# Performance work log

Hardware: AMD Instinct MI355X
Metric: run time of the kernel (lower is better)

## Reference

```python
import jax, jax.numpy as jnp
import numpy as np

DN = ('NCHW', 'OIHW', 'NCHW')
B, C, H, W = 4, 64, 256, 256
MIP = 8          # max(8, C // 32)
RED = C // 16    # CBAM reduced channels
PS = 8           # FSAS patch size


def conv2d(x, w, padding=0, groups=1):
    return jax.lax.conv_general_dilated(
        x, w, (1, 1), [(padding, padding), (padding, padding)],
        dimension_numbers=DN, feature_group_count=groups)


def bn_eval(x, g, b, eps=1e-5):
    # BatchNorm with init running stats (mean=0, var=1), eval mode
    return x / jnp.sqrt(1.0 + eps) * g[None, :, None, None] + b[None, :, None, None]


def h_swish(x):
    return x * jnp.clip(x + 3.0, 0.0, 6.0) / 6.0


def setup_inputs() -> dict:
    key = jax.random.key(0)
    ks = jax.random.split(key, 12)
    s = 0.05
    d = {
        'x': jax.random.normal(ks[0], (B, C, H, W), jnp.float32),
        # CoordAttention
        'ca_conv1_w': jax.random.normal(ks[1], (MIP, C, 1, 1), jnp.float32) * s,
        'ca_conv1_b': jnp.zeros((MIP,), jnp.float32),
        'ca_bn_g': jnp.ones((MIP,), jnp.float32),
        'ca_bn_b': jnp.zeros((MIP,), jnp.float32),
        'ca_convh_w': jax.random.normal(ks[2], (C, MIP, 1, 1), jnp.float32) * s,
        'ca_convh_b': jnp.zeros((C,), jnp.float32),
        'ca_convw_w': jax.random.normal(ks[3], (C, MIP, 1, 1), jnp.float32) * s,
        'ca_convw_b': jnp.zeros((C,), jnp.float32),
        # FSAS (bias=False)
        'fsas_hidden_w': jax.random.normal(ks[4], (6 * C, C, 1, 1), jnp.float32) * s,
        'fsas_dw_w': jax.random.normal(ks[5], (6 * C, 1, 3, 3), jnp.float32) * s,
        'fsas_proj_w': jax.random.normal(ks[6], (C, 2 * C, 1, 1), jnp.float32) * s,
        'ln_w': jnp.ones((2 * C,), jnp.float32),
        'ln_b': jnp.zeros((2 * C,), jnp.float32),
        # Fusion
        'fus_conv1_w': jax.random.normal(ks[7], (2 * C, 2 * C, 3, 3), jnp.float32) * s,
        'fus_bn1_g': jnp.ones((2 * C,), jnp.float32),
        'fus_bn1_b': jnp.zeros((2 * C,), jnp.float32),
        'fus_conv2_w': jax.random.normal(ks[8], (C, 2 * C, 1, 1), jnp.float32) * s,
        'fus_bn2_g': jnp.ones((C,), jnp.float32),
        'fus_bn2_b': jnp.zeros((C,), jnp.float32),
        # CBAM
        'cbam_mlp1_w': jax.random.normal(ks[9], (RED, C, 1, 1), jnp.float32) * s,
        'cbam_mlp2_w': jax.random.normal(ks[10], (C, RED, 1, 1), jnp.float32) * s,
        'cbam_sa_w': jax.random.normal(ks[11], (1, 2, 7, 7), jnp.float32) * s,
        'residual_scale': jnp.float32(0.1),
    }
    return d


def _forward(x, ca_conv1_w, ca_conv1_b, ca_bn_g, ca_bn_b, ca_convh_w, ca_convh_b,
             ca_convw_w, ca_convw_b, fsas_hidden_w, fsas_dw_w, fsas_proj_w, ln_w, ln_b,
             fus_conv1_w, fus_bn1_g, fus_bn1_b, fus_conv2_w, fus_bn2_g, fus_bn2_b,
             cbam_mlp1_w, cbam_mlp2_w, cbam_sa_w, residual_scale):
    b, c, h, w = x.shape
    c2 = 2 * c

    # ---- CoordAttention branch ----
    xh = jnp.mean(x, axis=3, keepdims=True)                       # [B,C,H,1]
    xw = jnp.mean(x, axis=2, keepdims=True).transpose(0, 1, 3, 2)  # [B,C,W,1]
    y = jnp.concatenate([xh, xw], axis=2)                          # [B,C,H+W,1]
    y = conv2d(y, ca_conv1_w) + ca_conv1_b[None, :, None, None]
    y = h_swish(bn_eval(y, ca_bn_g, ca_bn_b))
    yh, yw = y[:, :, :h], y[:, :, h:]
    yw = yw.transpose(0, 1, 3, 2)
    a_h = jax.nn.sigmoid(conv2d(yh, ca_convh_w) + ca_convh_b[None, :, None, None])
    a_w = jax.nn.sigmoid(conv2d(yw, ca_convw_w) + ca_convw_b[None, :, None, None])
    ca_out = x * a_h * a_w

    # ---- FSAS branch ----
    hid = conv2d(x, fsas_hidden_w)                                 # [B,6C,H,W]
    hid = conv2d(hid, fsas_dw_w, padding=1, groups=6 * c)          # depthwise 3x3
    q, k, v = jnp.split(hid, 3, axis=1)                            # each [B,2C,H,W]

    def patch(t):  # [B,2C,H,W] -> [B,2C,H/8,W/8,8,8]
        return t.reshape(b, c2, h // PS, PS, w // PS, PS).transpose(0, 1, 2, 4, 3, 5)

    qf = jnp.fft.rfft2(patch(q))
    kf = jnp.fft.rfft2(patch(k))
    o = jnp.fft.irfft2(qf * kf, s=(PS, PS))
    o = o.transpose(0, 1, 2, 4, 3, 5).reshape(b, c2, h, w)

    # WithBias LayerNorm over channel dim (per pixel)
    mu = jnp.mean(o, axis=1, keepdims=True)
    var = jnp.var(o, axis=1, keepdims=True)
    on = (o - mu) / jnp.sqrt(var + 1e-5) * ln_w[None, :, None, None] + ln_b[None, :, None, None]
    fsas_out = conv2d(v * on, fsas_proj_w)                         # [B,C,H,W]

    # ---- Fusion ----
    f = conv2d(jnp.concatenate([ca_out, fsas_out], axis=1), fus_conv1_w, padding=1)
    f = jax.nn.gelu(bn_eval(f, fus_bn1_g, fus_bn1_b), approximate=False)
    f = bn_eval(conv2d(f, fus_conv2_w), fus_bn2_g, fus_bn2_b)

    z = x + residual_scale * f

    # ---- CBAM ----
    avg = jnp.mean(z, axis=(2, 3), keepdims=True)
    mx = jnp.max(z, axis=(2, 3), keepdims=True)

    def mlp(t):
        return conv2d(jax.nn.relu(conv2d(t, cbam_mlp1_w)), cbam_mlp2_w)

    z = z * jax.nn.sigmoid(mlp(avg) + mlp(mx))
    sa = jnp.concatenate([jnp.mean(z, axis=1, keepdims=True),
                          jnp.max(z, axis=1, keepdims=True)], axis=1)
    z = z * jax.nn.sigmoid(conv2d(sa, cbam_sa_w, padding=3))
    return jax.nn.gelu(z, approximate=False)


def reference(x, ca_conv1_w, ca_conv1_b, ca_bn_g, ca_bn_b, ca_convh_w, ca_convh_b,
              ca_convw_w, ca_convw_b, fsas_hidden_w, fsas_dw_w, fsas_proj_w, ln_w, ln_b,
              fus_conv1_w, fus_bn1_g, fus_bn1_b, fus_conv2_w, fus_bn2_g, fus_bn2_b,
              cbam_mlp1_w, cbam_mlp2_w, cbam_sa_w, residual_scale):
    return _forward(x, ca_conv1_w, ca_conv1_b, ca_bn_g, ca_bn_b, ca_convh_w, ca_convh_b,
                    ca_convw_w, ca_convw_b, fsas_hidden_w, fsas_dw_w, fsas_proj_w, ln_w, ln_b,
                    fus_conv1_w, fus_bn1_g, fus_bn1_b, fus_conv2_w, fus_bn2_g, fus_bn2_b,
                    cbam_mlp1_w, cbam_mlp2_w, cbam_sa_w, residual_scale)
```

## Files before the change

kernel.cpp:

```cpp
#include <hip/hip_runtime.h>
#include <math.h>

#define B_ 4
#define C_ 64
#define C2_ 128
#define C6_ 384
#define H_ 256
#define Wd_ 256
#define HW_ 65536
#define MIP_ 8
#define BNINV 0.9999950000374994f

typedef short bf16x8 __attribute__((ext_vector_type(8)));
typedef float f32x4 __attribute__((ext_vector_type(4)));
typedef unsigned short u16x8 __attribute__((ext_vector_type(8)));
typedef unsigned short u16x4 __attribute__((ext_vector_type(4)));
typedef unsigned int   u32x4 __attribute__((ext_vector_type(4)));

__device__ __forceinline__ float sigm(float x){ return 1.f/(1.f+expf(-x)); }
__device__ __forceinline__ float gelu_f(float x){ return 0.5f*x*(1.f+erff(x*0.7071067811865476f)); }
__device__ __forceinline__ unsigned short bfrnd(float f){
  unsigned u = __float_as_uint(f);
  unsigned r = u + 0x7FFFu + ((u>>16)&1u);
  return (unsigned short)(r>>16);
}
__device__ __forceinline__ float bf2f(unsigned short s){
  return __uint_as_float(((unsigned)s)<<16);
}

__global__ void k_rowmean(const float* __restrict__ x, float* __restrict__ xh){
  int row = blockIdx.x*4 + (threadIdx.x>>6);
  int lane = threadIdx.x & 63;
  const float* p = x + (size_t)row*Wd_;
  float s = p[lane]+p[lane+64]+p[lane+128]+p[lane+192];
  #pragma unroll
  for(int off=32; off>0; off>>=1) s += __shfl_down(s, off, 64);
  if(lane==0) xh[row] = s*(1.f/Wd_);
}

__global__ void k_colmean(const float* __restrict__ x, float* __restrict__ xw){
  int idx = blockIdx.x*256 + threadIdx.x;
  int w = idx & 255; int bc = idx >> 8;
  const float* p = x + (size_t)bc*HW_ + w;
  float s = 0.f;
  for(int h=0;h<H_;h++) s += p[h*Wd_];
  xw[idx] = s*(1.f/H_);
}

__global__ void k_ca_t(const float* __restrict__ xh, const float* __restrict__ xw,
                       const float* __restrict__ w1, const float* __restrict__ b1,
                       const float* __restrict__ bng, const float* __restrict__ bnb,
                       float* __restrict__ t){
  int idx = blockIdx.x*256 + threadIdx.x;
  int p = idx & 511; int m = (idx>>9)&7; int b = idx>>12;
  float acc = b1[m];
  #pragma unroll 8
  for(int c=0;c<C_;c++){
    float yv = (p<256) ? xh[(b*C_+c)*256 + p] : xw[(b*C_+c)*256 + (p-256)];
    acc += w1[m*C_+c]*yv;
  }
  float v = acc*BNINV*bng[m] + bnb[m];
  t[idx] = v * fminf(fmaxf(v+3.f,0.f),6.f)*(1.f/6.f);
}

__global__ void k_ca_a(const float* __restrict__ t,
                       const float* __restrict__ wh, const float* __restrict__ bh,
                       const float* __restrict__ ww, const float* __restrict__ bw,
                       float* __restrict__ ah, float* __restrict__ aw){
  int idx = blockIdx.x*256 + threadIdx.x;
  int p = idx & 511; int co = (idx>>9)&63; int b = idx>>15;
  bool isH = (p<256);
  const float* wm = isH ? wh : ww;
  float acc = isH ? bh[co] : bw[co];
  #pragma unroll
  for(int m=0;m<MIP_;m++) acc += wm[co*MIP_+m]*t[(b*MIP_+m)*512+p];
  float s = sigm(acc);
  if(isH) ah[(b*C_+co)*256+p] = s; else aw[(b*C_+co)*256+(p-256)] = s;
}

__global__ void __launch_bounds__(256) k_xprep(const float* __restrict__ x, unsigned short* __restrict__ xb){
  __shared__ float sm[64][65];
  int tid = threadIdx.x;
  int img = blockIdx.x >> 10;
  int p0 = (blockIdx.x & 1023)*64;
  int lane = tid & 63, wq = tid >> 6;
  #pragma unroll
  for(int cc=0; cc<16; ++cc){
    int c = cc*4 + wq;
    sm[c][lane] = x[(size_t)(img*C_+c)*HW_ + p0 + lane];
  }
  __syncthreads();
  int pl = tid >> 2;
  int c0 = (tid & 3) * 16;
  u16x8 lo, hi;
  #pragma unroll
  for(int i=0;i<8;i++)  lo[i] = bfrnd(sm[c0+i][pl]);
  #pragma unroll
  for(int i=0;i<8;i++)  hi[i] = bfrnd(sm[c0+8+i][pl]);
  unsigned short* dst = xb + ((size_t)img*HW_ + p0 + pl)*64 + c0;
  *(u16x8*)(dst)     = lo;
  *(u16x8*)(dst + 8) = hi;
}

__global__ void k_wprep(const float* __restrict__ w, unsigned short* __restrict__ wbt){
  int t = blockIdx.x*256 + threadIdx.x;
  const float* src = w + (size_t)t*9;
  int oc = t >> 7, ic = t & 127;
  #pragma unroll
  for(int tap=0; tap<9; ++tap)
    wbt[(size_t)(tap*128+oc)*128 + ic] = bfrnd(src[tap]);
}

__global__ void k_wprep2(const float* __restrict__ pw, const float* __restrict__ w2,
                         const float* __restrict__ hw, unsigned short* __restrict__ pwb,
                         unsigned short* __restrict__ w2b, unsigned short* __restrict__ wb1){
  int t = blockIdx.x*256 + threadIdx.x;
  if(t < 8192){ pwb[t] = bfrnd(pw[t]); w2b[t] = bfrnd(w2[t]); }
  wb1[t] = bfrnd(hw[t]);
}

__global__ void __launch_bounds__(256) k_hid0_mfma(const unsigned short* __restrict__ xb,
                                                   const unsigned short* __restrict__ wb1,
                                                   unsigned short* __restrict__ hid0b){
  int tid = threadIdx.x;
  int lane = tid & 63, wid = tid >> 6;
  int l15 = lane & 15, lk = lane >> 4;
  int p0 = blockIdx.x*128 + wid*32;
  int oc0 = blockIdx.y*96;
  f32x4 acc[6][2];
  #pragma unroll
  for(int m=0;m<6;m++)
    #pragma unroll
    for(int n=0;n<2;n++) acc[m][n] = (f32x4)0.f;
  #pragma unroll
  for(int kk=0; kk<2; ++kk){
    bf16x8 bfr[2];
    #pragma unroll
    for(int n=0;n<2;n++)
      bfr[n] = *(const bf16x8*)(xb + (size_t)(p0 + n*16 + l15)*64 + kk*32 + lk*8);
    #pragma unroll
    for(int m=0;m<6;m++){
      bf16x8 af = *(const bf16x8*)(wb1 + (size_t)(oc0 + m*16 + l15)*64 + kk*32 + lk*8);
      #pragma unroll
      for(int n=0;n<2;n++)
        acc[m][n] = __builtin_amdgcn_mfma_f32_16x16x32_bf16(af, bfr[n], acc[m][n], 0,0,0);
    }
  }
  #pragma unroll
  for(int n=0;n<2;n++){
    int p = p0 + n*16 + l15;
    #pragma unroll
    for(int m=0;m<6;m++){
      u16x4 v;
      #pragma unroll
      for(int r=0;r<4;r++) v[r] = bfrnd(acc[m][n][r]);
      *(u16x4*)(hid0b + (size_t)p*384 + oc0 + m*16 + lk*4) = v;
    }
  }
}

__global__ void __launch_bounds__(256) k_dw_bf(const unsigned short* __restrict__ hid0b,
                                               const float* __restrict__ wd,
                                               unsigned short* __restrict__ hidb){
  int tid = threadIdx.x;
  int cg = tid & 15;
  int tg = tid >> 4;
  int p0 = blockIdx.x*64;
  int h  = p0 >> 8;
  int w0 = (p0 & 255) + tg*4;
  int chb = blockIdx.y*128 + cg*8;

  float wreg[72];
  {
    const f32x4* wsrc = (const f32x4*)(wd + (size_t)chb*9);
    #pragma unroll
    for(int i=0;i<18;i++){
      f32x4 v = wsrc[i];
      wreg[4*i+0]=v[0]; wreg[4*i+1]=v[1]; wreg[4*i+2]=v[2]; wreg[4*i+3]=v[3];
    }
  }
  float acc[4][8];
  #pragma unroll
  for(int px=0;px<4;px++)
    #pragma unroll
    for(int e=0;e<8;e++) acc[px][e] = 0.f;

  #pragma unroll
  for(int ky=0; ky<3; ++ky){
    int hh = h + ky - 1;
    if((unsigned)hh >= 256u) continue;
    float row[6][8];
    #pragma unroll
    for(int c6=0; c6<6; ++c6){
      int ww = w0 + c6 - 1;
      u16x8 v8 = {0,0,0,0,0,0,0,0};
      if((unsigned)ww < 256u)
        v8 = *(const u16x8*)(hid0b + (size_t)(hh*256+ww)*384 + chb);
      #pragma unroll
      for(int e=0;e<8;e++) row[c6][e] = bf2f(v8[e]);
    }
    #pragma unroll
    for(int kx=0; kx<3; ++kx){
      #pragma unroll
      for(int px=0; px<4; ++px){
        #pragma unroll
        for(int e=0;e<8;e++)
          acc[px][e] += row[px+kx][e] * wreg[e*9 + ky*3 + kx];
      }
    }
  }
  #pragma unroll
  for(int px=0; px<4; ++px){
    u16x8 o8;
    #pragma unroll
    for(int e=0;e<8;e++) o8[e] = bfrnd(acc[px][e]);
    *(u16x8*)(hidb + (size_t)(p0 + tg*4 + px)*384 + chb) = o8;
  }
}

__global__ void __launch_bounds__(256) k_circ_bf(const unsigned short* __restrict__ hidb,
                                                 unsigned short* __restrict__ ob){
  __shared__ __align__(16) unsigned short lq[2][64][128];
  __shared__ __align__(16) unsigned short lkk[2][64][128];
  int tid = threadIdx.x;
  #pragma unroll
  for(int it=0; it<8; ++it){
    int s = it*256 + tid;
    int which = s >> 10, rem = s & 1023;
    int pix = rem >> 4, cg = rem & 15;
    int gp = blockIdx.x*2 + which;
    int ph = gp >> 5, pw = gp & 31;
    size_t pg = (size_t)((ph*8 + (pix>>3))*256 + pw*8 + (pix&7));
    *(u16x8*)&lq[which][pix][cg*8]  = *(const u16x8*)(hidb + pg*384 + cg*8);
    *(u16x8*)&lkk[which][pix][cg*8] = *(const u16x8*)(hidb + pg*384 + 128 + cg*8);
  }
  __syncthreads();
  int which = tid >> 7, c = tid & 127;
  float kr[64];
  #pragma unroll
  for(int pix=0;pix<64;pix++) kr[pix] = bf2f(lkk[which][pix][c]);
  float outv[64];
  #pragma unroll
  for(int t2=0;t2<64;t2++) outv[t2] = 0.f;
  #pragma unroll
  for(int u=0;u<8;u++){
    #pragma unroll
    for(int v=0;v<8;v++){
      float qv = bf2f(lq[which][u*8+v][c]);
      #pragma unroll
      for(int i=0;i<8;i++){
        #pragma unroll
        for(int j=0;j<8;j++)
          outv[i*8+j] += qv * kr[((i-u)&7)*8 + ((j-v)&7)];
      }
    }
  }
  __syncthreads();
  #pragma unroll
  for(int t2=0;t2<64;t2++) lq[which][t2][c] = bfrnd(outv[t2]);
  __syncthreads();
  #pragma unroll
  for(int it=0; it<8; ++it){
    int s = it*256 + tid;
    int which2 = s >> 10, rem = s & 1023;
    int pix = rem >> 4, cg = rem & 15;
    int gp = blockIdx.x*2 + which2;
    int ph = gp >> 5, pw = gp & 31;
    size_t pg = (size_t)((ph*8 + (pix>>3))*256 + pw*8 + (pix&7));
    *(u16x8*)(ob + pg*128 + cg*8) = *(u16x8*)&lq[which2][pix][cg*8];
  }
}

__global__ void __launch_bounds__(256) k_proj_mfma(const unsigned short* __restrict__ ob,
                      const unsigned short* __restrict__ hidb,
                      const float* __restrict__ lnw, const float* __restrict__ lnb,
                      const unsigned short* __restrict__ pwb, unsigned short* __restrict__ catb){
  __shared__ unsigned int lds32[256*64];
  int tid = threadIdx.x;
  int lane = tid & 63, wid = tid >> 6;
  int p0 = blockIdx.x*256;
  {
    int p = p0 + tid;
    u16x8 o8[16];
    #pragma unroll
    for(int g=0; g<16; ++g) o8[g] = *(const u16x8*)(ob + (size_t)p*128 + g*8);
    float s=0.f, s2=0.f;
    #pragma unroll
    for(int g=0; g<16; ++g)
      #pragma unroll
      for(int e=0; e<8; ++e){ float v = bf2f(o8[g][e]); s += v; s2 += v*v; }
    float m = s*(1.f/C2_);
    float var = s2*(1.f/C2_) - m*m;
    float rs = rsqrtf(var + 1e-5f);
    #pragma unroll
    for(int cg=0; cg<16; ++cg){
      u16x8 v8 = *(const u16x8*)(hidb + (size_t)p*384 + 256 + cg*8);
      unsigned uu[4];
      #pragma unroll
      for(int ee=0; ee<4; ++ee){
        int c = cg*8 + ee*2;
        float on0 = (bf2f(o8[cg][2*ee])   - m)*rs*lnw[c]   + lnb[c];
        float on1 = (bf2f(o8[cg][2*ee+1]) - m)*rs*lnw[c+1] + lnb[c+1];
        float vn0 = bf2f(v8[2*ee])*on0;
        float vn1 = bf2f(v8[2*ee+1])*on1;
        uu[ee] = (unsigned)bfrnd(vn0) | ((unsigned)bfrnd(vn1)<<16);
      }
      int blk = cg ^ (tid & 15);
      u32x4 w4 = {uu[0],uu[1],uu[2],uu[3]};
      *(u32x4*)&lds32[tid*64 + blk*4] = w4;
    }
  }
  __syncthreads();
  int l15 = lane & 15, lk = lane >> 4;
  f32x4 acc[4][4];
  #pragma unroll
  for(int m=0;m<4;m++)
    #pragma unroll
    for(int n=0;n<4;n++) acc[m][n] = (f32x4)0.f;
  int plb = wid*64;
  #pragma unroll
  for(int kk=0; kk<4; ++kk){
    bf16x8 bfr[4];
    #pragma unroll
    for(int n=0;n<4;n++){
      int pl = plb + n*16 + l15;
      int blk = (kk*4 + lk) ^ l15;
      bfr[n] = *(bf16x8*)&lds32[pl*64 + blk*4];
    }
    #pragma unroll
    for(int m=0;m<4;m++){
      bf16x8 af = *(const bf16x8*)(pwb + (size_t)(m*16+l15)*128 + kk*32 + lk*8);
      #pragma unroll
      for(int n=0;n<4;n++)
        acc[m][n] = __builtin_amdgcn_mfma_f32_16x16x32_bf16(af, bfr[n], acc[m][n], 0,0,0);
    }
  }
  #pragma unroll
  for(int n=0;n<4;n++){
    int p = p0 + plb + n*16 + l15;
    #pragma unroll
    for(int m=0;m<4;m++){
      u16x4 v;
      #pragma unroll
      for(int r=0;r<4;r++) v[r] = bfrnd(acc[m][n][r]);
      *(u16x4*)(catb + (size_t)p*128 + 64 + m*16 + lk*4) = v;
    }
  }
}

__global__ void __launch_bounds__(256) k_caout_bf(const float* __restrict__ x, const float* __restrict__ ah,
                        const float* __restrict__ aw, unsigned short* __restrict__ catb, int b){
  __shared__ float sm[64][65];
  int tid = threadIdx.x;
  int p0 = blockIdx.x*64;
  int h = p0 >> 8;
  int wbase = p0 & 255;
  int lane = tid & 63, wq = tid >> 6;
  #pragma unroll
  for(int cc=0; cc<16; ++cc){
    int c = cc*4 + wq;
    float v = x[(size_t)(b*C_+c)*HW_ + p0 + lane];
    v *= ah[(b*C_+c)*256 + h] * aw[(b*C_+c)*256 + wbase + lane];
    sm[c][lane] = v;
  }
  __syncthreads();
  int pl = tid >> 2;
  int c0 = (tid & 3) * 16;
  u16x8 lo, hi;
  #pragma unroll
  for(int i=0;i<8;i++)  lo[i] = bfrnd(sm[c0+i][pl]);
  #pragma unroll
  for(int i=0;i<8;i++)  hi[i] = bfrnd(sm[c0+8+i][pl]);
  unsigned short* dst = catb + (size_t)(p0+pl)*128 + c0;
  *(u16x8*)(dst)     = lo;
  *(u16x8*)(dst + 8) = hi;
}

__global__ void __launch_bounds__(256,3) k_fus1_mfma(const unsigned short* __restrict__ catb,
                                                     const unsigned short* __restrict__ wbt,
                                                     unsigned short* __restrict__ f1b){
  __shared__ __align__(16) unsigned short sA[3][130][32];
  int tid = threadIdx.x;
  int lane = tid & 63, wid = tid >> 6;
  int wm = wid & 1, wn = wid >> 1;
  int bid = blockIdx.x;
  int xcd = bid & 7, idx = bid >> 3;
  int h   = xcd*32 + (idx >> 2);
  int w0  = ((idx >> 1) & 1) * 128;
  int ocb = (idx & 1) * 64 + wn*32;
  int l15 = lane & 15, lk = lane >> 4;

  int srow[7], spxl[7], sicq[7];
  bool sok[7], sld[7];
  #pragma unroll
  for(int it=0; it<7; ++it){
    int s = it*256 + tid;
    sok[it] = (s < 1560);
    int row = s/520;
    int rem = s - row*520;
    int pxl = rem >> 2;
    int icq = rem & 3;
    srow[it]=row; spxl[it]=pxl; sicq[it]=icq;
    int r = h + row - 1;
    int c = w0 + pxl - 1;
    sld[it] = sok[it] && (unsigned)r < 256u && (unsigned)c < 256u;
  }

  u16x8 st[7];
  #pragma unroll
  for(int it=0; it<7; ++it){
    u16x8 v = {0,0,0,0,0,0,0,0};
    if(sld[it]){
      int r = h + srow[it] - 1, c = w0 + spxl[it] - 1;
      v = *(const u16x8*)(catb + (size_t)(r*256 + c)*128 + sicq[it]*8);
    }
    st[it] = v;
  }

  f32x4 acc[4][2];
  #pragma unroll
  for(int i=0;i<4;i++)
    #pragma unroll
    for(int j=0;j<2;j++) acc[i][j] = (f32x4)0.f;

  const unsigned short* wbase = wbt + (size_t)(ocb + l15)*128 + lk*8;

  for(int icc=0; icc<4; ++icc){
    int ic0 = icc*32;
    __syncthreads();
    #pragma unroll
    for(int it=0; it<7; ++it){
      if(sok[it]){
        int blk = sicq[it] ^ ((spxl[it]>>1)&3);
        *(u16x8*)&sA[srow[it]][spxl[it]][blk*8] = st[it];
      }
    }
    __syncthreads();
    if(icc < 3){
      int ic0n = (icc+1)*32;
      #pragma unroll
      for(int it=0; it<7; ++it){
        u16x8 v = {0,0,0,0,0,0,0,0};
        if(sld[it]){
          int r = h + srow[it] - 1, c = w0 + spxl[it] - 1;
          v = *(const u16x8*)(catb + (size_t)(r*256 + c)*128 + ic0n + sicq[it]*8);
        }
        st[it] = v;
      }
    }
    #pragma unroll
    for(int ky=0; ky<3; ++ky){
      bf16x8 wf[3][2];
      #pragma unroll
      for(int kx=0; kx<3; ++kx){
        const unsigned short* wt = wbase + (size_t)(ky*3+kx)*16384 + ic0;
        wf[kx][0] = *(const bf16x8*)(wt);
        wf[kx][1] = *(const bf16x8*)(wt + 2048);
      }
      #pragma unroll
      for(int kx=0; kx<3; ++kx){
        #pragma unroll
        for(int i=0;i<4;++i){
          int rr = wm*64 + i*16 + l15 + kx;
          int blk = lk ^ ((rr>>1)&3);
          bf16x8 a = *(const bf16x8*)&sA[ky][rr][blk*8];
          acc[i][0] = __builtin_amdgcn_mfma_f32_16x16x32_bf16(wf[kx][0], a, acc[i][0], 0,0,0);
          acc[i][1] = __builtin_amdgcn_mfma_f32_16x16x32_bf16(wf[kx][1], a, acc[i][1], 0,0,0);
        }
      }
    }
  }
  #pragma unroll
  for(int i=0;i<4;i++){
    int sp = h*256 + w0 + wm*64 + i*16 + l15;
    #pragma unroll
    for(int j=0;j<2;j++){
      u16x4 v;
      #pragma unroll
      for(int r2=0;r2<4;r2++) v[r2] = bfrnd(acc[i][j][r2]);
      *(u16x4*)(f1b + (size_t)sp*128 + ocb + j*16 + lk*4) = v;
    }
  }
}

__global__ void __launch_bounds__(256) k_fus2_mfma(const unsigned short* __restrict__ f1b,
                      const float* __restrict__ x, const unsigned short* __restrict__ w2b,
                      const float* __restrict__ bn1g, const float* __restrict__ bn1b,
                      const float* __restrict__ bn2g, const float* __restrict__ bn2b,
                      const float* __restrict__ rscale, float* __restrict__ z,
                      float* __restrict__ psum2, float* __restrict__ pmax2, int b){
  __shared__ unsigned int lds32[128*64];
  __shared__ float smp[4][4][16], smm[4][4][16];
  int tid = threadIdx.x;
  int lane = tid & 63, wid = tid >> 6;
  int p0 = blockIdx.x*128;
  int ic0 = (tid & 15) * 8;
  #pragma unroll
  for(int pass=0; pass<8; ++pass){
    int pl = pass*16 + (tid>>4);
    bf16x8 vv = *(const bf16x8*)(f1b + (size_t)(p0+pl)*128 + ic0);
    unsigned uu[4];
    #pragma unroll
    for(int ee=0; ee<4; ++ee){
      float f0 = bf2f((unsigned short)vv[2*ee])  *BNINV*bn1g[ic0+2*ee]   + bn1b[ic0+2*ee];
      float f1 = bf2f((unsigned short)vv[2*ee+1])*BNINV*bn1g[ic0+2*ee+1] + bn1b[ic0+2*ee+1];
      uu[ee] = (unsigned)bfrnd(gelu_f(f0)) | ((unsigned)bfrnd(gelu_f(f1))<<16);
    }
    int blk = (ic0>>3) ^ (pl&15);
    u32x4 w4 = {uu[0],uu[1],uu[2],uu[3]};
    *(u32x4*)&lds32[pl*64 + blk*4] = w4;
  }
  __syncthreads();
  int l15 = lane & 15, lk = lane >> 4;
  f32x4 acc[4][2];
  #pragma unroll
  for(int m=0;m<4;m++)
    #pragma unroll
    for(int n=0;n<2;n++) acc[m][n] = (f32x4)0.f;
  int pl0 = wid*32 + l15;
  #pragma unroll
  for(int kk=0; kk<4; ++kk){
    bf16x8 bfr[2];
    #pragma unroll
    for(int n=0;n<2;n++){
      int pl = pl0 + n*16;
      int blk = (kk*4 + lk) ^ l15;
      bfr[n] = *(bf16x8*)&lds32[pl*64 + blk*4];
    }
    #pragma unroll
    for(int m=0;m<4;m++){
      bf16x8 af = *(const bf16x8*)(w2b + (size_t)(m*16+l15)*128 + kk*32 + lk*8);
      #pragma unroll
      for(int n=0;n<2;n++)
        acc[m][n] = __builtin_amdgcn_mfma_f32_16x16x32_bf16(af, bfr[n], acc[m][n], 0,0,0);
    }
  }
  float rs = rscale[0];
  float ps[4][4], pm[4][4];
  #pragma unroll
  for(int m=0;m<4;m++)
    #pragma unroll
    for(int r=0;r<4;r++){ ps[m][r]=0.f; pm[m][r]=-INFINITY; }
  #pragma unroll
  for(int n=0;n<2;n++){
    int p = p0 + pl0 + n*16;
    #pragma unroll
    for(int m=0;m<4;m++){
      #pragma unroll
      for(int r=0;r<4;r++){
        int oc = m*16 + lk*4 + r;
        float f = acc[m][n][r]*BNINV*bn2g[oc] + bn2b[oc];
        float zv = x[(size_t)(b*C_+oc)*HW_ + p] + rs*f;
        z[(size_t)oc*HW_ + p] = zv;
        ps[m][r] += zv; pm[m][r] = fmaxf(pm[m][r], zv);
      }
    }
  }
  #pragma unroll
  for(int off=1; off<16; off<<=1){
    #pragma unroll
    for(int m=0;m<4;m++)
      #pragma unroll
      for(int r=0;r<4;r++){
        ps[m][r] += __shfl_xor(ps[m][r], off, 64);
        pm[m][r] = fmaxf(pm[m][r], __shfl_xor(pm[m][r], off, 64));
      }
  }
  if(l15 == 0){
    #pragma unroll
    for(int m=0;m<4;m++)
      #pragma unroll
      for(int r=0;r<4;r++){
        smp[wid][lk][m*4+r] = ps[m][r];
        smm[wid][lk][m*4+r] = pm[m][r];
      }
  }
  __syncthreads();
  if(tid < 64){
    int m = tid>>4, lkg = (tid>>2)&3, r = tid&3;
    float s = 0.f, mx = -INFINITY;
    #pragma unroll
    for(int w=0;w<4;w++){
      s += smp[w][lkg][m*4+r];
      mx = fmaxf(mx, smm[w][lkg][m*4+r]);
    }
    psum2[blockIdx.x*64 + tid] = s;
    pmax2[blockIdx.x*64 + tid] = mx;
  }
}

__global__ void k_cbamred2(const float* __restrict__ psum2, const float* __restrict__ pmax2,
                           float* __restrict__ avgb, float* __restrict__ maxb){
  int c = blockIdx.x; int tid = threadIdx.x;
  float s = psum2[(size_t)tid*64 + c] + psum2[(size_t)(tid+256)*64 + c];
  float m = fmaxf(pmax2[(size_t)tid*64 + c], pmax2[(size_t)(tid+256)*64 + c]);
  __shared__ float ss[256], sm[256];
  ss[tid]=s; sm[tid]=m; __syncthreads();
  for(int off=128; off>0; off>>=1){
    if(tid<off){ ss[tid]+=ss[tid+off]; sm[tid]=fmaxf(sm[tid],sm[tid+off]); }
    __syncthreads();
  }
  if(tid==0){ avgb[c]=ss[0]*(1.f/HW_); maxb[c]=sm[0]; }
}

__global__ void k_cbammlp(const float* __restrict__ avgb, const float* __restrict__ maxb,
                          const float* __restrict__ w1, const float* __restrict__ w2,
                          float* __restrict__ catt){
  __shared__ float h1s[8];
  int tid = threadIdx.x;
  if(tid<8){
    const float* src = (tid<4)? avgb : maxb;
    int r = tid & 3;
    float s = 0.f;
    for(int c=0;c<C_;c++) s += w1[r*C_+c]*src[c];
    h1s[tid] = fmaxf(s,0.f);
  }
  __syncthreads();
  float a = 0.f;
  #pragma unroll
  for(int r=0;r<4;r++) a += w2[tid*4+r]*(h1s[r]+h1s[r+4]);
  catt[tid] = sigm(a);
}

__global__ void k_chatt(const float* __restrict__ z, const float* __restrict__ catt,
                        float* __restrict__ samean, float* __restrict__ samax){
  int p = blockIdx.x*256 + threadIdx.x;
  float s = 0.f, m = -INFINITY;
  #pragma unroll 8
  for(int c=0;c<C_;c++){
    float v = z[(size_t)c*HW_+p]*catt[c];
    s += v; m = fmaxf(m,v);
  }
  samean[p] = s*(1.f/C_);
  samax[p] = m;
}

__global__ void k_saconv(const float* __restrict__ samean, const float* __restrict__ samax,
                         const float* __restrict__ saw, float* __restrict__ att){
  int p = blockIdx.x*256 + threadIdx.x;
  int h = p>>8, w = p&255;
  float acc = 0.f;
  #pragma unroll
  for(int ky=0;ky<7;ky++){
    int hh = h+ky-3; if((unsigned)hh>=256u) continue;
    #pragma unroll
    for(int kx=0;kx<7;kx++){
      int ww2 = w+kx-3; if((unsigned)ww2>=256u) continue;
      int q = hh*256+ww2;
      acc += samean[q]*saw[ky*7+kx] + samax[q]*saw[49+ky*7+kx];
    }
  }
  att[p] = sigm(acc);
}

__global__ void k_final(const float* __restrict__ z, const float* __restrict__ catt,
                        const float* __restrict__ att, float* __restrict__ out, int b){
  int p = blockIdx.x*256 + threadIdx.x;
  int c = blockIdx.y;
  float v = z[(size_t)c*HW_+p]*catt[c]*att[p];
  out[(size_t)(b*C_+c)*HW_+p] = gelu_f(v);
}

extern "C" void kernel_launch(void* const* d_in, const int* in_sizes, int n_in,
                              void* d_out, int out_size, void* d_ws, size_t ws_size,
                              hipStream_t stream){
  const float* x            = (const float*)d_in[0];
  const float* ca_conv1_w   = (const float*)d_in[1];
  const float* ca_conv1_b   = (const float*)d_in[2];
  const float* ca_bn_g      = (const float*)d_in[3];
  const float* ca_bn_b      = (const float*)d_in[4];
  const float* ca_convh_w   = (const float*)d_in[5];
  const float* ca_convh_b   = (const float*)d_in[6];
  const float* ca_convw_w   = (const float*)d_in[7];
  const float* ca_convw_b   = (const float*)d_in[8];
  const float* fsas_hidden_w= (const float*)d_in[9];
  const float* fsas_dw_w    = (const float*)d_in[10];
  const float* fsas_proj_w  = (const float*)d_in[11];
  const float* ln_w         = (const float*)d_in[12];
  const float* ln_b         = (const float*)d_in[13];
  const float* fus_conv1_w  = (const float*)d_in[14];
  const float* fus_bn1_g    = (const float*)d_in[15];
  const float* fus_bn1_b    = (const float*)d_in[16];
  const float* fus_conv2_w  = (const float*)d_in[17];
  const float* fus_bn2_g    = (const float*)d_in[18];
  const float* fus_bn2_b    = (const float*)d_in[19];
  const float* cbam_mlp1_w  = (const float*)d_in[20];
  const float* cbam_mlp2_w  = (const float*)d_in[21];
  const float* cbam_sa_w    = (const float*)d_in[22];
  const float* rscale       = (const float*)d_in[23];
  float* out = (float*)d_out;
  float* ws  = (float*)d_ws;

  float* xh     = ws + 0;
  float* xw     = ws + 65536;
  float* t      = ws + 131072;
  float* ah     = ws + 147456;
  float* aw     = ws + 212992;
  float* catt   = ws + 278528;
  float* avgb   = ws + 278592;
  float* maxb   = ws + 278656;
  float* psum2  = ws + 278720;
  float* pmax2  = ws + 311488;
  float* samean = ws + 344256;
  float* samax  = ws + 409792;
  float* att    = ws + 475328;
  float* big    = ws + 540864;
  unsigned short* catb  = (unsigned short*)(big);
  unsigned short* f1b   = (unsigned short*)(big + 4194304);
  float*          z     =                  big + 8388608;
  unsigned short* xb    = (unsigned short*)(big + 12582912);
  unsigned short* hid0b = (unsigned short*)(big + 20971520);
  unsigned short* hidb  = (unsigned short*)(big + 33554432);
  unsigned short* obuf  = (unsigned short*)(big + 46137344);
  unsigned short* wbt   = (unsigned short*)(big + 50331648);
  unsigned short* wb1   = (unsigned short*)(big + 50405376);
  unsigned short* pwb   = (unsigned short*)(big + 50417664);
  unsigned short* w2b   = (unsigned short*)(big + 50421760);

  k_rowmean<<<16384,256,0,stream>>>(x, xh);
  k_colmean<<<256,256,0,stream>>>(x, xw);
  k_ca_t<<<64,256,0,stream>>>(xh, xw, ca_conv1_w, ca_conv1_b, ca_bn_g, ca_bn_b, t);
  k_ca_a<<<512,256,0,stream>>>(t, ca_convh_w, ca_convh_b, ca_convw_w, ca_convw_b, ah, aw);
  k_xprep<<<4096,256,0,stream>>>(x, xb);
  k_wprep<<<64,256,0,stream>>>(fus_conv1_w, wbt);
  k_wprep2<<<96,256,0,stream>>>(fsas_proj_w, fus_conv2_w, fsas_hidden_w, pwb, w2b, wb1);

  for(int b=0;b<4;b++){
    k_hid0_mfma<<<dim3(512,4),256,0,stream>>>(xb + (size_t)b*HW_*64, wb1, hid0b);
    k_dw_bf<<<dim3(1024,3),256,0,stream>>>(hid0b, fsas_dw_w, hidb);
    k_circ_bf<<<512,256,0,stream>>>(hidb, obuf);
    k_proj_mfma<<<256,256,0,stream>>>(obuf, hidb, ln_w, ln_b, pwb, catb);
    k_caout_bf<<<1024,256,0,stream>>>(x, ah, aw, catb, b);
    k_fus1_mfma<<<1024,256,0,stream>>>(catb, wbt, f1b);
    k_fus2_mfma<<<512,256,0,stream>>>(f1b, x, w2b, fus_bn1_g, fus_bn1_b, fus_bn2_g, fus_bn2_b,
                                      rscale, z, psum2, pmax2, b);
    k_cbamred2<<<64,256,0,stream>>>(psum2, pmax2, avgb, maxb);
    k_cbammlp<<<1,64,0,stream>>>(avgb, maxb, cbam_mlp1_w, cbam_mlp2_w, catt);
    k_chatt<<<256,256,0,stream>>>(z, catt, samean, samax);
    k_saconv<<<256,256,0,stream>>>(samean, samax, cbam_sa_w, att);
    k_final<<<dim3(256,64),256,0,stream>>>(z, catt, att, out, b);
  }
}
```

Baseline: 824.9 us.

## Store z in bf16, batch CBAM tail across images, merge row/col mean kernels

The intermediate z tensor is now stored as bf16 for all four images instead of an fp32 per-image buffer, which halves its write and read traffic. The CBAM reduction, MLP, channel-attention, spatial-conv and final kernels move out of the per-batch loop and run once over all four images, giving larger grids and fewer launches. The separate row-mean and column-mean kernels become a single per-plane kernel. Rounding z to bf16 adds precision loss in the output path, and the larger z buffer raises workspace size.

Measured after the change: 766.6 us. -7.1%, faster.

```diff
diff --git a/kernel.cpp b/kernel.cpp
--- a/kernel.cpp
+++ b/kernel.cpp
@@ -28,23 +28,19 @@
   return __uint_as_float(((unsigned)s)<<16);
 }
 
-__global__ void k_rowmean(const float* __restrict__ x, float* __restrict__ xh){
-  int row = blockIdx.x*4 + (threadIdx.x>>6);
-  int lane = threadIdx.x & 63;
-  const float* p = x + (size_t)row*Wd_;
-  float s = p[lane]+p[lane+64]+p[lane+128]+p[lane+192];
-  #pragma unroll
-  for(int off=32; off>0; off>>=1) s += __shfl_down(s, off, 64);
-  if(lane==0) xh[row] = s*(1.f/Wd_);
-}
-
-__global__ void k_colmean(const float* __restrict__ x, float* __restrict__ xw){
-  int idx = blockIdx.x*256 + threadIdx.x;
-  int w = idx & 255; int bc = idx >> 8;
-  const float* p = x + (size_t)bc*HW_ + w;
-  float s = 0.f;
-  for(int h=0;h<H_;h++) s += p[h*Wd_];
-  xw[idx] = s*(1.f/H_);
+__global__ void __launch_bounds__(256) k_xstat(const float* __restrict__ x,
+                                               float* __restrict__ xh, float* __restrict__ xw){
+  int plane = blockIdx.x;
+  int tid = threadIdx.x;
+  const float* p = x + (size_t)plane*HW_;
+  float cs = 0.f;
+  for(int h=0;h<256;h++) cs += p[h*256+tid];
+  xw[plane*256+tid] = cs*(1.f/256.f);
+  float rs = 0.f;
+  const f32x4* pr4 = (const f32x4*)(p + (size_t)tid*256);
+  #pragma unroll 8
+  for(int w=0;w<64;w++){ f32x4 v = pr4[w]; rs += v[0]+v[1]+v[2]+v[3]; }
+  xh[plane*256+tid] = rs*(1.f/256.f);
 }
 
 __global__ void k_ca_t(const float* __restrict__ xh, const float* __restrict__ xw,
@@ -487,7 +483,7 @@
                       const float* __restrict__ x, const unsigned short* __restrict__ w2b,
                       const float* __restrict__ bn1g, const float* __restrict__ bn1b,
                       const float* __restrict__ bn2g, const float* __restrict__ bn2b,
-                      const float* __restrict__ rscale, float* __restrict__ z,
+                      const float* __restrict__ rscale, unsigned short* __restrict__ zb,
                       float* __restrict__ psum2, float* __restrict__ pmax2, int b){
   __shared__ unsigned int lds32[128*64];
   __shared__ float smp[4][4][16], smm[4][4][16];
@@ -551,7 +547,7 @@
         int oc = m*16 + lk*4 + r;
         float f = acc[m][n][r]*BNINV*bn2g[oc] + bn2b[oc];
         float zv = x[(size_t)(b*C_+oc)*HW_ + p] + rs*f;
-        z[(size_t)oc*HW_ + p] = zv;
+        zb[(size_t)oc*HW_ + p] = bfrnd(zv);
         ps[m][r] += zv; pm[m][r] = fmaxf(pm[m][r], zv);
       }
     }
@@ -590,54 +586,63 @@
 }
 
 __global__ void k_cbamred2(const float* __restrict__ psum2, const float* __restrict__ pmax2,
-                           float* __restrict__ avgb, float* __restrict__ maxb){
-  int c = blockIdx.x; int tid = threadIdx.x;
-  float s = psum2[(size_t)tid*64 + c] + psum2[(size_t)(tid+256)*64 + c];
-  float m = fmaxf(pmax2[(size_t)tid*64 + c], pmax2[(size_t)(tid+256)*64 + c]);
+                           float* __restrict__ avgb4, float* __restrict__ maxb4){
+  int c = blockIdx.x & 63; int b = blockIdx.x >> 6;
+  const float* ps = psum2 + (size_t)b*32768;
+  const float* pmx = pmax2 + (size_t)b*32768;
+  int tid = threadIdx.x;
+  float s = ps[(size_t)tid*64 + c] + ps[(size_t)(tid+256)*64 + c];
+  float m = fmaxf(pmx[(size_t)tid*64 + c], pmx[(size_t)(tid+256)*64 + c]);
   __shared__ float ss[256], sm[256];
   ss[tid]=s; sm[tid]=m; __syncthreads();
   for(int off=128; off>0; off>>=1){
     if(tid<off){ ss[tid]+=ss[tid+off]; sm[tid]=fmaxf(sm[tid],sm[tid+off]); }
     __syncthreads();
   }
-  if(tid==0){ avgb[c]=ss[0]*(1.f/HW_); maxb[c]=sm[0]; }
-}
-
-__global__ void k_cbammlp(const float* __restrict__ avgb, const float* __restrict__ maxb,
+  if(tid==0){ avgb4[b*64+c]=ss[0]*(1.f/HW_); maxb4[b*64+c]=sm[0]; }
+}
+
+__global__ void k_cbammlp(const float* __restrict__ avgb4, const float* __restrict__ maxb4,
                           const float* __restrict__ w1, const float* __restrict__ w2,
-                          float* __restrict__ catt){
-  __shared__ float h1s[8];
-  int tid = threadIdx.x;
-  if(tid<8){
-    const float* src = (tid<4)? avgb : maxb;
-    int r = tid & 3;
+                          float* __restrict__ catt4){
+  __shared__ float h1s[4][8];
+  int tid = threadIdx.x;
+  int b = tid >> 6, cl = tid & 63;
+  if(cl < 8){
+    const float* src = (cl<4)? avgb4 + b*64 : maxb4 + b*64;
+    int r = cl & 3;
     float s = 0.f;
     for(int c=0;c<C_;c++) s += w1[r*C_+c]*src[c];
-    h1s[tid] = fmaxf(s,0.f);
+    h1s[b][cl] = fmaxf(s,0.f);
   }
   __syncthreads();
   float a = 0.f;
   #pragma unroll
-  for(int r=0;r<4;r++) a += w2[tid*4+r]*(h1s[r]+h1s[r+4]);
-  catt[tid] = sigm(a);
-}
-
-__global__ void k_chatt(const float* __restrict__ z, const float* __restrict__ catt,
-                        float* __restrict__ samean, float* __restrict__ samax){
-  int p = blockIdx.x*256 + threadIdx.x;
+  for(int r=0;r<4;r++) a += w2[cl*4+r]*(h1s[b][r]+h1s[b][r+4]);
+  catt4[b*64+cl] = sigm(a);
+}
+
+__global__ void k_chatt(const unsigned short* __restrict__ z4, const float* __restrict__ catt4,
+                        float* __restrict__ samean4, float* __restrict__ samax4){
+  int gp = blockIdx.x*256 + threadIdx.x;
+  int b = gp >> 16; int p = gp & 65535;
+  const unsigned short* zb = z4 + (size_t)b*C_*HW_;
+  const float* ct = catt4 + b*64;
   float s = 0.f, m = -INFINITY;
   #pragma unroll 8
   for(int c=0;c<C_;c++){
-    float v = z[(size_t)c*HW_+p]*catt[c];
+    float v = bf2f(zb[(size_t)c*HW_+p])*ct[c];
     s += v; m = fmaxf(m,v);
   }
-  samean[p] = s*(1.f/C_);
-  samax[p] = m;
-}
-
-__global__ void k_saconv(const float* __restrict__ samean, const float* __restrict__ samax,
-                         const float* __restrict__ saw, float* __restrict__ att){
-  int p = blockIdx.x*256 + threadIdx.x;
+  samean4[gp] = s*(1.f/C_);
+  samax4[gp] = m;
+}
+
+__global__ void k_saconv(const float* __restrict__ samean4, const float* __restrict__ samax4,
+                         const float* __restrict__ saw, float* __restrict__ att4){
+  int gp = blockIdx.x*256 + threadIdx.x;
+  int b = gp >> 16; int p = gp & 65535;
+  int base = b << 16;
   int h = p>>8, w = p&255;
   float acc = 0.f;
   #pragma unroll
@@ -646,19 +651,20 @@
     #pragma unroll
     for(int kx=0;kx<7;kx++){
       int ww2 = w+kx-3; if((unsigned)ww2>=256u) continue;
-      int q = hh*256+ww2;
-      acc += samean[q]*saw[ky*7+kx] + samax[q]*saw[49+ky*7+kx];
-    }
-  }
-  att[p] = sigm(acc);
-}
-
-__global__ void k_final(const float* __restrict__ z, const float* __restrict__ catt,
-                        const float* __restrict__ att, float* __restrict__ out, int b){
-  int p = blockIdx.x*256 + threadIdx.x;
+      int q = base + hh*256+ww2;
+      acc += samean4[q]*saw[ky*7+kx] + samax4[q]*saw[49+ky*7+kx];
+    }
+  }
+  att4[gp] = sigm(acc);
+}
+
+__global__ void k_final(const unsigned short* __restrict__ z4, const float* __restrict__ catt4,
+                        const float* __restrict__ att4, float* __restrict__ out){
+  int gp = blockIdx.x*256 + threadIdx.x;
+  int b = gp >> 16; int p = gp & 65535;
   int c = blockIdx.y;
-  float v = z[(size_t)c*HW_+p]*catt[c]*att[p];
-  out[(size_t)(b*C_+c)*HW_+p] = gelu_f(v);
+  float v = bf2f(z4[((size_t)(b*C_+c))*HW_ + p]) * catt4[b*64+c] * att4[gp];
+  out[((size_t)(b*C_+c))*HW_ + p] = gelu_f(v);
 }
 
 extern "C" void kernel_launch(void* const* d_in, const int* in_sizes, int n_in,
@@ -691,34 +697,33 @@
   float* out = (float*)d_out;
   float* ws  = (float*)d_ws;
 
-  float* xh     = ws + 0;
-  float* xw     = ws + 65536;
-  float* t      = ws + 131072;
-  float* ah     = ws + 147456;
-  float* aw     = ws + 212992;
-  float* catt   = ws + 278528;
-  float* avgb   = ws + 278592;
-  float* maxb   = ws + 278656;
-  float* psum2  = ws + 278720;
-  float* pmax2  = ws + 311488;
-  float* samean = ws + 344256;
-  float* samax  = ws + 409792;
-  float* att    = ws + 475328;
-  float* big    = ws + 540864;
+  float* xh      = ws + 0;
+  float* xw      = ws + 65536;
+  float* t       = ws + 131072;
+  float* ah      = ws + 147456;
+  float* aw      = ws + 212992;
+  float* catt4   = ws + 278528;
+  float* avgb4   = ws + 278784;
+  float* maxb4   = ws + 279040;
+  float* psum2   = ws + 279296;
+  float* pmax2   = ws + 410368;
+  float* samean4 = ws + 541440;
+  float* samax4  = ws + 803584;
+  float* att4    = ws + 1065728;
+  float* big     = ws + 1327872;
   unsigned short* catb  = (unsigned short*)(big);
   unsigned short* f1b   = (unsigned short*)(big + 4194304);
-  float*          z     =                  big + 8388608;
-  unsigned short* xb    = (unsigned short*)(big + 12582912);
-  unsigned short* hid0b = (unsigned short*)(big + 20971520);
-  unsigned short* hidb  = (unsigned short*)(big + 33554432);
-  unsigned short* obuf  = (unsigned short*)(big + 46137344);
-  unsigned short* wbt   = (unsigned short*)(big + 50331648);
-  unsigned short* wb1   = (unsigned short*)(big + 50405376);
-  unsigned short* pwb   = (unsigned short*)(big + 50417664);
-  unsigned short* w2b   = (unsigned short*)(big + 50421760);
-
-  k_rowmean<<<16384,256,0,stream>>>(x, xh);
-  k_colmean<<<256,256,0,stream>>>(x, xw);
+  unsigned short* z4    = (unsigned short*)(big + 8388608);
+  unsigned short* xb    = (unsigned short*)(big + 16777216);
+  unsigned short* hid0b = (unsigned short*)(big + 25165824);
+  unsigned short* hidb  = (unsigned short*)(big + 37748736);
+  unsigned short* obuf  = (unsigned short*)(big + 50331648);
+  unsigned short* wbt   = (unsigned short*)(big + 54525952);
+  unsigned short* wb1   = (unsigned short*)(big + 54599680);
+  unsigned short* pwb   = (unsigned short*)(big + 54611968);
+  unsigned short* w2b   = (unsigned short*)(big + 54616064);
+
+  k_xstat<<<256,256,0,stream>>>(x, xh, xw);
   k_ca_t<<<64,256,0,stream>>>(xh, xw, ca_conv1_w, ca_conv1_b, ca_bn_g, ca_bn_b, t);
   k_ca_a<<<512,256,0,stream>>>(t, ca_convh_w, ca_convh_b, ca_convw_w, ca_convw_b, ah, aw);
   k_xprep<<<4096,256,0,stream>>>(x, xb);
@@ -733,11 +738,13 @@
     k_caout_bf<<<1024,256,0,stream>>>(x, ah, aw, catb, b);
     k_fus1_mfma<<<1024,256,0,stream>>>(catb, wbt, f1b);
     k_fus2_mfma<<<512,256,0,stream>>>(f1b, x, w2b, fus_bn1_g, fus_bn1_b, fus_bn2_g, fus_bn2_b,
-                                      rscale, z, psum2, pmax2, b);
-    k_cbamred2<<<64,256,0,stream>>>(psum2, pmax2, avgb, maxb);
-    k_cbammlp<<<1,64,0,stream>>>(avgb, maxb, cbam_mlp1_w, cbam_mlp2_w, catt);
-    k_chatt<<<256,256,0,stream>>>(z, catt, samean, samax);
-    k_saconv<<<256,256,0,stream>>>(samean, samax, cbam_sa_w, att);
-    k_final<<<dim3(256,64),256,0,stream>>>(z, catt, att, out, b);
-  }
-}
+                                      rscale, z4 + (size_t)b*C_*HW_,
+                                      psum2 + (size_t)b*32768, pmax2 + (size_t)b*32768, b);
+  }
+
+  k_cbamred2<<<256,256,0,stream>>>(psum2, pmax2, avgb4, maxb4);
+  k_cbammlp<<<1,256,0,stream>>>(avgb4, maxb4, cbam_mlp1_w, cbam_mlp2_w, catt4);
+  k_chatt<<<1024,256,0,stream>>>(z4, catt4, samean4, samax4);
+  k_saconv<<<1024,256,0,stream>>>(samean4, samax4, cbam_sa_w, att4);
+  k_final<<<dim3(1024,64),256,0,stream>>>(z4, catt4, att4, out);
+}
```
